# Optimization experiments

Hardware: AMD Instinct MI355X
Metric: run time of the kernel (lower is better)

The kernel has to match this reference:

```python
import jax, jax.numpy as jnp
import numpy as np

N_HEADS = 16

def setup_inputs() -> dict:
    key = jax.random.key(0)
    ks = jax.random.split(key, 8)
    bs, t, h, dh = 32, 512, 1024, 64
    s = lambda k, shape: jax.random.normal(k, shape, dtype=jnp.float32) * 0.02
    return {
        "x": jax.random.normal(ks[0], (bs, t, h), dtype=jnp.float32),
        "Wq": s(ks[1], (h, h)),
        "bq": s(ks[2], (h,)),
        "Wk": s(ks[3], (h, h)),
        "bk": s(ks[4], (h,)),
        "Wv": s(ks[5], (h, dh)),
        "bv": s(ks[6], (dh,)),
        "Wo": s(ks[7], (dh, h)),
    }

def reference(x, Wq, bq, Wk, bk, Wv, bv, Wo):
    bs, t, h = x.shape
    dh = Wv.shape[1]
    nh = N_HEADS
    # projections (context == x; static_features=None path)
    q = (x @ Wq + bq).reshape(bs, t, nh, dh)   # [b,t,h,d]
    k = (x @ Wk + bk).reshape(bs, t, nh, dh)
    v = x @ Wv + bv                             # shared single-head V: [b,t,d]
    scale = dh ** -0.5
    # per-head scores [b,h,q,k]
    score = jnp.einsum('bqhd,bkhd->bhqk', q, k) * scale
    # causal mask (mask_future_timesteps=True): -inf above diagonal
    mask = jnp.triu(jnp.full((t, t), -jnp.inf, dtype=score.dtype), 1)
    score = score + mask
    prob = jax.nn.softmax(score, axis=-1)       # attn_dropout is identity (p=0)
    # broadcast shared V across heads
    attn_vec = jnp.einsum('bhqk,bkd->bhqd', prob, v)   # [b,h,t,d]
    m_attn_vec = jnp.mean(attn_vec, axis=1)            # head-mean pooling [b,t,d]
    out = m_attn_vec @ Wo                              # out_proj, no bias; out_dropout identity
    return out, attn_vec
```

## Files before the change

kernel.cpp:

```cpp
#include <hip/hip_runtime.h>
#include <hip/hip_bf16.h>
#include <math.h>

#define BS 32
#define TT 512
#define HH 1024
#define NH 16
#define DH 64
#define MM (BS*TT)
#define NCAT 2176

typedef __attribute__((ext_vector_type(8))) __bf16 bf16x8;
typedef __attribute__((ext_vector_type(4))) float  f32x4;

#define QSCALE 0.18033688011112042f

#if __has_builtin(__builtin_amdgcn_exp2f)
#define EXP2F(x) __builtin_amdgcn_exp2f(x)
#else
#define EXP2F(x) __expf((x) * 0.69314718055994531f)
#endif

__device__ __forceinline__ void gld16(const void* g, void* l) {
    __builtin_amdgcn_global_load_lds(
        (const __attribute__((address_space(1))) unsigned int*)g,
        (__attribute__((address_space(3))) unsigned int*)l,
        16, 0, 0);
}

__global__ __launch_bounds__(256) void cvt_x(const float* __restrict__ x,
                                             __bf16* __restrict__ xb)
{
    const size_t i = ((size_t)blockIdx.x * 256 + threadIdx.x) * 8;
    float4 a = *(const float4*)(x + i);
    float4 b = *(const float4*)(x + i + 4);
    bf16x8 v;
    v[0] = (__bf16)a.x; v[1] = (__bf16)a.y; v[2] = (__bf16)a.z; v[3] = (__bf16)a.w;
    v[4] = (__bf16)b.x; v[5] = (__bf16)b.y; v[6] = (__bf16)b.z; v[7] = (__bf16)b.w;
    *(bf16x8*)(xb + i) = v;
}

__global__ __launch_bounds__(256) void prep_w(
    const float* __restrict__ Wq, const float* __restrict__ Wk,
    const float* __restrict__ Wv, const float* __restrict__ bq_,
    const float* __restrict__ bk_, const float* __restrict__ bv_,
    __bf16* __restrict__ Wt, float* __restrict__ bias_cat)
{
    __shared__ __align__(16) __bf16 tile[64][72];
    const int tid = threadIdx.x;
    const int n0 = blockIdx.x * 64;
    const int k0 = blockIdx.y * 64;

    const int n_l = tid & 63;
    const int k_b = tid >> 6;
    const int n   = n0 + n_l;
    #pragma unroll
    for (int j = 0; j < 16; ++j) {
        const int k_l = j * 4 + k_b;
        const int k   = k0 + k_l;
        float v;
        if (n < 1024)      v = Wq[(size_t)k * 1024 + n];
        else if (n < 2048) v = Wk[(size_t)k * 1024 + (n - 1024)];
        else if (n < 2112) v = Wv[(size_t)k * 64 + (n - 2048)];
        else               v = 0.f;
        tile[n_l][k_l] = (__bf16)v;
    }
    if (blockIdx.y == 0 && tid < 64) {
        const int nn = n0 + tid;
        bias_cat[nn] = (nn < 1024) ? bq_[nn]
                     : (nn < 2048) ? bk_[nn - 1024]
                     : (nn < 2112) ? bv_[nn - 2048] : 0.f;
    }
    __syncthreads();
    const int n_l2 = tid >> 2;
    const int k_l2 = (tid & 3) * 16;
    __bf16* dst = Wt + (size_t)(n0 + n_l2) * 1024 + k0 + k_l2;
    *(bf16x8*)dst       = *(const bf16x8*)&tile[n_l2][k_l2];
    *(bf16x8*)(dst + 8) = *(const bf16x8*)&tile[n_l2][k_l2 + 8];
}

__global__ __launch_bounds__(256) void gemm_qkv(
    const __bf16* __restrict__ A, const __bf16* __restrict__ B,
    const float* __restrict__ bias_cat,
    __bf16* __restrict__ Qo, __bf16* __restrict__ Ko,
    __bf16* __restrict__ Vt)
{
    __shared__ __align__(16) __bf16 sA[128 * 32];
    __shared__ __align__(16) __bf16 sB[128 * 32];

    const int tid  = threadIdx.x;
    const int wv   = tid >> 6;
    const int ln   = tid & 63;
    const int quad = ln >> 4;
    const int l16  = ln & 15;

    const int orig = blockIdx.y * 17 + blockIdx.x;
    const int swz  = (orig & 7) * 272 + (orig >> 3);
    const int m0 = (swz / 17) * 128;
    const int n0 = (swz % 17) * 128;

    const int rw = (wv & 1) * 64;
    const int cw = (wv >> 1) * 64;

    f32x4 acc[4][4];
    #pragma unroll
    for (int i = 0; i < 4; ++i)
        #pragma unroll
        for (int j = 0; j < 4; ++j) acc[i][j] = f32x4{0, 0, 0, 0};

    const int srow = wv * 16 + (ln >> 2);
    const int scol = (ln & 3) * 8;
    const __bf16* ga0 = A + (size_t)(m0 + srow) * 1024 + scol;
    const __bf16* gb0 = B + (size_t)(n0 + srow) * 1024 + scol;
    __bf16* la0 = sA + wv * 512;
    __bf16* lb0 = sB + wv * 512;

    for (int k0 = 0; k0 < 1024; k0 += 32) {
        gld16(ga0 + k0, la0);
        gld16(ga0 + (size_t)64 * 1024 + k0, la0 + 2048);
        gld16(gb0 + k0, lb0);
        gld16(gb0 + (size_t)64 * 1024 + k0, lb0 + 2048);
        __syncthreads();

        bf16x8 af[4], bfr[4];
        #pragma unroll
        for (int mt = 0; mt < 4; ++mt)
            af[mt] = *(const bf16x8*)&sA[(rw + mt * 16 + l16) * 32 + quad * 8];
        #pragma unroll
        for (int nt = 0; nt < 4; ++nt)
            bfr[nt] = *(const bf16x8*)&sB[(cw + nt * 16 + l16) * 32 + quad * 8];
        #pragma unroll
        for (int mt = 0; mt < 4; ++mt)
            #pragma unroll
            for (int nt = 0; nt < 4; ++nt)
                acc[mt][nt] = __builtin_amdgcn_mfma_f32_16x16x32_bf16(af[mt], bfr[nt], acc[mt][nt], 0, 0, 0);
        __syncthreads();
    }

    #pragma unroll
    for (int mt = 0; mt < 4; ++mt) {
        #pragma unroll
        for (int nt = 0; nt < 4; ++nt) {
            const int colb = n0 + cw + nt * 16 + l16;
            if (colb >= 2112) continue;
            const float bias = bias_cat[colb];
            #pragma unroll
            for (int r = 0; r < 4; ++r) {
                const int row = m0 + rw + mt * 16 + quad * 4 + r;
                const int b = row >> 9, t = row & 511;
                float v = acc[mt][nt][r] + bias;
                if (colb < 1024) {
                    const int h = colb >> 6, d = colb & 63;
                    Qo[(((size_t)(b * NH + h) * TT) + t) * DH + d] = (__bf16)(v * QSCALE);
                } else if (colb < 2048) {
                    const int c = colb - 1024;
                    const int h = c >> 6, d = c & 63;
                    Ko[(((size_t)(b * NH + h) * TT) + t) * DH + d] = (__bf16)v;
                } else {
                    const int d = colb - 2048;
                    Vt[((size_t)(b * DH + d)) * TT + t] = (__bf16)v;
                }
            }
        }
    }
}

__global__ __launch_bounds__(1024) void attn_mfma(
    const __bf16* __restrict__ Q, const __bf16* __restrict__ K,
    const __bf16* __restrict__ Vt, float* __restrict__ attn_vec)
{
    __shared__ __align__(16) __bf16 sK[512 * 64];
    __shared__ __align__(16) __bf16 sV[64][512];

    const int bh   = blockIdx.x;
    const int b    = bh >> 4;
    const int wave = threadIdx.x >> 6;
    const int lane = threadIdx.x & 63;
    const int quad = lane >> 4;
    const int l16  = lane & 15;

    const int s_ = wave & 3, j_ = wave >> 2;
    const int qt2 = (j_ == 0) ? s_ : (j_ == 1) ? (7 - s_) : (j_ == 2) ? (8 + s_) : (15 - s_);
    const int q0   = qt2 << 5;
    const int kend = q0 + 32;

    const __bf16* Qbh = Q + (size_t)bh * TT * DH;
    const __bf16* Kbh = K + (size_t)bh * TT * DH;
    const __bf16* Vb  = Vt + (size_t)b * DH * TT;

    #pragma unroll
    for (int r = 0; r < 4; ++r) {
        const int c   = wave * 4 + r;
        const int row = c * 8 + (lane >> 3);
        const int p   = lane & 7;
        const int swz = (row & 3) | (((row >> 3) & 1) << 2);
        gld16(Kbh + (size_t)row * DH + ((p ^ swz) * 8), sK + (size_t)c * 512);
    }
    const int svw = wave & 7;
    #pragma unroll
    for (int r = 0; r < 4; ++r) {
        const int row = wave + r * 16;
        gld16(Vb + (size_t)row * TT + ((lane ^ svw) * 8), &sV[row][0]);
    }

    const bf16x8 qA_lo = *(const bf16x8*)(Qbh + (size_t)(q0 + l16) * DH + quad * 8);
    const bf16x8 qA_hi = *(const bf16x8*)(Qbh + (size_t)(q0 + l16) * DH + 32 + quad * 8);
    const bf16x8 qB_lo = *(const bf16x8*)(Qbh + (size_t)(q0 + 16 + l16) * DH + quad * 8);
    const bf16x8 qB_hi = *(const bf16x8*)(Qbh + (size_t)(q0 + 16 + l16) * DH + 32 + quad * 8);

    const int perm = ((l16 >> 2) << 3) + (l16 & 3);
    const int swzl = (l16 & 3) | (((l16 >> 2) & 1) << 2);
    const __bf16* k1lo = sK + (size_t)perm * DH       + (( quad      ^ swzl) * 8);
    const __bf16* k1hi = sK + (size_t)perm * DH       + (((quad | 4) ^ swzl) * 8);
    const __bf16* k2lo = sK + (size_t)(perm + 4) * DH + (( quad      ^ swzl) * 8);
    const __bf16* k2hi = sK + (size_t)(perm + 4) * DH + (((quad | 4) ^ swzl) * 8);

    const int sx = l16 & 7;

    f32x4 OA[4] = {f32x4{0,0,0,0}, f32x4{0,0,0,0}, f32x4{0,0,0,0}, f32x4{0,0,0,0}};
    f32x4 OB[4] = {f32x4{0,0,0,0}, f32x4{0,0,0,0}, f32x4{0,0,0,0}, f32x4{0,0,0,0}};
    float lA = 0.f, lB = 0.f;

    __syncthreads();

    for (int kb0 = 0; kb0 < kend; kb0 += 32) {
        const int ko = kb0 * DH;
        bf16x8 c1a = *(const bf16x8*)(k1lo + ko);
        bf16x8 c1b = *(const bf16x8*)(k1hi + ko);
        bf16x8 c2a = *(const bf16x8*)(k2lo + ko);
        bf16x8 c2b = *(const bf16x8*)(k2hi + ko);

        const int vg = (((kb0 >> 3) + quad) ^ sx) * 8;
        bf16x8 vf0 = *(const bf16x8*)&sV[l16][vg];
        bf16x8 vf1 = *(const bf16x8*)&sV[16 + l16][vg];
        bf16x8 vf2 = *(const bf16x8*)&sV[32 + l16][vg];
        bf16x8 vf3 = *(const bf16x8*)&sV[48 + l16][vg];

        f32x4 s1A = __builtin_amdgcn_mfma_f32_16x16x32_bf16(c1a, qA_lo, f32x4{0,0,0,0}, 0, 0, 0);
        s1A       = __builtin_amdgcn_mfma_f32_16x16x32_bf16(c1b, qA_hi, s1A, 0, 0, 0);
        f32x4 s2A = __builtin_amdgcn_mfma_f32_16x16x32_bf16(c2a, qA_lo, f32x4{0,0,0,0}, 0, 0, 0);
        s2A       = __builtin_amdgcn_mfma_f32_16x16x32_bf16(c2b, qA_hi, s2A, 0, 0, 0);
        f32x4 s1B = __builtin_amdgcn_mfma_f32_16x16x32_bf16(c1a, qB_lo, f32x4{0,0,0,0}, 0, 0, 0);
        s1B       = __builtin_amdgcn_mfma_f32_16x16x32_bf16(c1b, qB_hi, s1B, 0, 0, 0);
        f32x4 s2B = __builtin_amdgcn_mfma_f32_16x16x32_bf16(c2a, qB_lo, f32x4{0,0,0,0}, 0, 0, 0);
        s2B       = __builtin_amdgcn_mfma_f32_16x16x32_bf16(c2b, qB_hi, s2B, 0, 0, 0);

        if (kb0 == q0) {
            const int qqA = q0 + l16, qqB = q0 + 16 + l16;
            #pragma unroll
            for (int r = 0; r < 4; ++r) {
                const int key1 = kb0 + quad * 8 + r;
                const int key2 = key1 + 4;
                if (key1 > qqA) s1A[r] = -INFINITY;
                if (key2 > qqA) s2A[r] = -INFINITY;
                if (key1 > qqB) s1B[r] = -INFINITY;
                if (key2 > qqB) s2B[r] = -INFINITY;
            }
        }

        bf16x8 pfA, pfB;
        float psA0 = 0.f, psA1 = 0.f, psB0 = 0.f, psB1 = 0.f;
        #pragma unroll
        for (int r = 0; r < 4; ++r) {
            float pa0 = EXP2F(s1A[r]);
            float pa1 = EXP2F(s2A[r]);
            float pb0 = EXP2F(s1B[r]);
            float pb1 = EXP2F(s2B[r]);
            psA0 += pa0; psA1 += pa1;
            psB0 += pb0; psB1 += pb1;
            pfA[r]     = (__bf16)pa0;
            pfA[4 + r] = (__bf16)pa1;
            pfB[r]     = (__bf16)pb0;
            pfB[4 + r] = (__bf16)pb1;
        }
        lA += psA0 + psA1;
        lB += psB0 + psB1;

        OA[0] = __builtin_amdgcn_mfma_f32_16x16x32_bf16(pfA, vf0, OA[0], 0, 0, 0);
        OB[0] = __builtin_amdgcn_mfma_f32_16x16x32_bf16(pfB, vf0, OB[0], 0, 0, 0);
        OA[1] = __builtin_amdgcn_mfma_f32_16x16x32_bf16(pfA, vf1, OA[1], 0, 0, 0);
        OB[1] = __builtin_amdgcn_mfma_f32_16x16x32_bf16(pfB, vf1, OB[1], 0, 0, 0);
        OA[2] = __builtin_amdgcn_mfma_f32_16x16x32_bf16(pfA, vf2, OA[2], 0, 0, 0);
        OB[2] = __builtin_amdgcn_mfma_f32_16x16x32_bf16(pfB, vf2, OB[2], 0, 0, 0);
        OA[3] = __builtin_amdgcn_mfma_f32_16x16x32_bf16(pfA, vf3, OA[3], 0, 0, 0);
        OB[3] = __builtin_amdgcn_mfma_f32_16x16x32_bf16(pfB, vf3, OB[3], 0, 0, 0);
    }

    lA += __shfl_xor(lA, 16);
    lA += __shfl_xor(lA, 32);
    lB += __shfl_xor(lB, 16);
    lB += __shfl_xor(lB, 32);

    #pragma unroll
    for (int r = 0; r < 4; ++r) {
        const float invA = 1.0f / __shfl(lA, quad * 4 + r);
        const float invB = 1.0f / __shfl(lB, quad * 4 + r);
        const int tA = q0 + quad * 4 + r;
        const int tB = tA + 16;
        float* opA = attn_vec + ((size_t)bh * TT + tA) * DH + l16;
        float* opB = attn_vec + ((size_t)bh * TT + tB) * DH + l16;
        #pragma unroll
        for (int nt = 0; nt < 4; ++nt) {
            opA[nt * 16] = OA[nt][r] * invA;
            opB[nt * 16] = OB[nt][r] * invB;
        }
    }
}

__global__ __launch_bounds__(256) void reduce_heads(
    const float* __restrict__ av, float* __restrict__ mav)
{
    const size_t idx = (size_t)blockIdx.x * 256 + threadIdx.x;
    const int    d4  = (int)(idx & 15);
    const size_t bt  = idx >> 4;
    const int    b   = (int)(bt >> 9);
    const int    t   = (int)(bt & 511);
    const float4* p = (const float4*)av + (((size_t)b * NH * TT) + t) * 16 + d4;
    float4 a = p[0];
    #pragma unroll
    for (int h = 1; h < NH; ++h) {
        float4 v = p[(size_t)h * TT * 16];
        a.x += v.x; a.y += v.y; a.z += v.z; a.w += v.w;
    }
    float4 o;
    o.x = a.x * (1.f / 16.f); o.y = a.y * (1.f / 16.f);
    o.z = a.z * (1.f / 16.f); o.w = a.w * (1.f / 16.f);
    ((float4*)mav)[idx] = o;
}

__global__ __launch_bounds__(256) void gemm_out(
    const float* __restrict__ A, const float* __restrict__ B,
    float* __restrict__ C, int M, int N, int K)
{
    __shared__ __align__(16) __bf16 sA[64][32];
    __shared__ __align__(16) __bf16 sB[64][32];

    const int tid  = threadIdx.x;
    const int wave = tid >> 6;
    const int lane = tid & 63;
    const int m0 = blockIdx.y * 64;
    const int n0 = blockIdx.x * 64;

    f32x4 acc[4] = {f32x4{0,0,0,0}, f32x4{0,0,0,0}, f32x4{0,0,0,0}, f32x4{0,0,0,0}};

    const int ar = tid >> 2;
    const int ac = (tid & 3) * 8;
    const int bk = tid >> 3;
    const int bc = (tid & 7) * 8;
    const int quad = lane >> 4;
    const int l16  = lane & 15;

    for (int k0 = 0; k0 < K; k0 += 32) {
        const float* ap = A + (size_t)(m0 + ar) * K + k0 + ac;
        float4 a0 = *(const float4*)ap;
        float4 a1 = *(const float4*)(ap + 4);
        {
            bf16x8 av;
            av[0] = (__bf16)a0.x; av[1] = (__bf16)a0.y; av[2] = (__bf16)a0.z; av[3] = (__bf16)a0.w;
            av[4] = (__bf16)a1.x; av[5] = (__bf16)a1.y; av[6] = (__bf16)a1.z; av[7] = (__bf16)a1.w;
            *(bf16x8*)&sA[ar][ac] = av;
        }
        const float* bp = B + (size_t)(k0 + bk) * N + n0 + bc;
        float4 b0 = *(const float4*)bp;
        float4 b1 = *(const float4*)(bp + 4);
        sB[bc + 0][bk] = (__bf16)b0.x;
        sB[bc + 1][bk] = (__bf16)b0.y;
        sB[bc + 2][bk] = (__bf16)b0.z;
        sB[bc + 3][bk] = (__bf16)b0.w;
        sB[bc + 4][bk] = (__bf16)b1.x;
        sB[bc + 5][bk] = (__bf16)b1.y;
        sB[bc + 6][bk] = (__bf16)b1.z;
        sB[bc + 7][bk] = (__bf16)b1.w;
        __syncthreads();

        bf16x8 afrag = *(const bf16x8*)&sA[wave * 16 + l16][quad * 8];
        #pragma unroll
        for (int tn = 0; tn < 4; ++tn) {
            bf16x8 bfrag = *(const bf16x8*)&sB[tn * 16 + l16][quad * 8];
            acc[tn] = __builtin_amdgcn_mfma_f32_16x16x32_bf16(afrag, bfrag, acc[tn], 0, 0, 0);
        }
        __syncthreads();
    }

    #pragma unroll
    for (int tn = 0; tn < 4; ++tn) {
        #pragma unroll
        for (int r = 0; r < 4; ++r) {
            int row = m0 + wave * 16 + quad * 4 + r;
            int col = n0 + tn * 16 + l16;
            C[(size_t)row * N + col] = acc[tn][r];
        }
    }
}

extern "C" void kernel_launch(void* const* d_in, const int* in_sizes, int n_in,
                              void* d_out, int out_size, void* d_ws, size_t ws_size,
                              hipStream_t stream)
{
    const float* x  = (const float*)d_in[0];
    const float* Wq = (const float*)d_in[1];
    const float* bq = (const float*)d_in[2];
    const float* Wk = (const float*)d_in[3];
    const float* bk = (const float*)d_in[4];
    const float* Wv = (const float*)d_in[5];
    const float* bv = (const float*)d_in[6];
    const float* Wo = (const float*)d_in[7];

    float* out      = (float*)d_out;
    float* attn_vec = out + (size_t)MM * HH;

    char* ws = (char*)d_ws;
    __bf16* xb  = (__bf16*)ws;
    __bf16* Wt  = xb + (size_t)MM * HH;
    float* bias_cat = (float*)(Wt + (size_t)NCAT * HH);
    __bf16* Qb  = (__bf16*)(bias_cat + 2304);
    __bf16* Kb  = Qb + (size_t)MM * HH;
    __bf16* Vt  = Kb + (size_t)MM * HH;
    float*  mav = (float*)xb;

    cvt_x<<<MM * HH / (256 * 8), 256, 0, stream>>>(x, xb);
    prep_w<<<dim3(NCAT / 64, HH / 64), 256, 0, stream>>>(Wq, Wk, Wv, bq, bk, bv, Wt, bias_cat);
    gemm_qkv<<<dim3(NCAT / 128, MM / 128), 256, 0, stream>>>(xb, Wt, bias_cat, Qb, Kb, Vt);
    attn_mfma<<<BS * NH, 1024, 0, stream>>>(Qb, Kb, Vt, attn_vec);
    reduce_heads<<<(MM * DH / 4) / 256, 256, 0, stream>>>(attn_vec, mav);
    gemm_out<<<dim3(HH / 64, MM / 64), 256, 0, stream>>>(mav, Wo, out, MM, HH, DH);
}
```

Measured before the change: 359.2 us.

## Double-buffer QKV GEMM with BK=64 swizzled LDS and rework output projection

The QKV GEMM now uses a K-step of 64 with XOR-swizzled LDS tiles and double buffering, so the next tile's global-to-LDS loads are issued while MFMAs run on the current tile, with one barrier per step. The head-mean reduction now writes bf16 directly, and Wo is pre-transposed to bf16 in a new small kernel. The output GEMM reads fragments straight from global memory without LDS and computes a larger 64x64 tile per wave. This adds LDS usage, which may lower occupancy in the QKV GEMM, and an extra launch.

```diff
diff --git a/kernel.cpp b/kernel.cpp
--- a/kernel.cpp
+++ b/kernel.cpp
@@ -79,14 +79,26 @@
     *(bf16x8*)(dst + 8) = *(const bf16x8*)&tile[n_l2][k_l2 + 8];
 }
 
+__global__ __launch_bounds__(256) void prep_wo(const float* __restrict__ Wo,
+                                               __bf16* __restrict__ WoT)
+{
+    const int idx = blockIdx.x * 256 + threadIdx.x;
+    const int n  = idx >> 3;
+    const int k0 = (idx & 7) * 8;
+    bf16x8 v;
+    #pragma unroll
+    for (int j = 0; j < 8; ++j) v[j] = (__bf16)Wo[(size_t)(k0 + j) * 1024 + n];
+    *(bf16x8*)(WoT + (size_t)n * 64 + k0) = v;
+}
+
 __global__ __launch_bounds__(256) void gemm_qkv(
     const __bf16* __restrict__ A, const __bf16* __restrict__ B,
     const float* __restrict__ bias_cat,
     __bf16* __restrict__ Qo, __bf16* __restrict__ Ko,
     __bf16* __restrict__ Vt)
 {
-    __shared__ __align__(16) __bf16 sA[128 * 32];
-    __shared__ __align__(16) __bf16 sB[128 * 32];
+    __shared__ __align__(16) __bf16 sA[2][128 * 64];
+    __shared__ __align__(16) __bf16 sB[2][128 * 64];
 
     const int tid  = threadIdx.x;
     const int wv   = tid >> 6;
@@ -108,33 +120,52 @@
         #pragma unroll
         for (int j = 0; j < 4; ++j) acc[i][j] = f32x4{0, 0, 0, 0};
 
-    const int srow = wv * 16 + (ln >> 2);
-    const int scol = (ln & 3) * 8;
-    const __bf16* ga0 = A + (size_t)(m0 + srow) * 1024 + scol;
-    const __bf16* gb0 = B + (size_t)(n0 + srow) * 1024 + scol;
-    __bf16* la0 = sA + wv * 512;
-    __bf16* lb0 = sB + wv * 512;
-
-    for (int k0 = 0; k0 < 1024; k0 += 32) {
-        gld16(ga0 + k0, la0);
-        gld16(ga0 + (size_t)64 * 1024 + k0, la0 + 2048);
-        gld16(gb0 + k0, lb0);
-        gld16(gb0 + (size_t)64 * 1024 + k0, lb0 + 2048);
+    const int srow8 = ln >> 3;
+    const int srcg  = (ln & 7) ^ (srow8 & 7);
+    const int swr   = (l16 & 7);
+
+    #pragma unroll
+    for (int r = 0; r < 4; ++r) {
+        const int rowb = wv * 32 + r * 8;
+        gld16(A + (size_t)(m0 + rowb + srow8) * 1024 + srcg * 8, &sA[0][rowb * 64]);
+        gld16(B + (size_t)(n0 + rowb + srow8) * 1024 + srcg * 8, &sB[0][rowb * 64]);
+    }
+    __syncthreads();
+
+    int p = 0;
+    for (int k0 = 0; k0 < 1024; k0 += 64) {
+        if (k0 + 64 < 1024) {
+            #pragma unroll
+            for (int r = 0; r < 4; ++r) {
+                const int rowb = wv * 32 + r * 8;
+                gld16(A + (size_t)(m0 + rowb + srow8) * 1024 + k0 + 64 + srcg * 8,
+                      &sA[p ^ 1][rowb * 64]);
+                gld16(B + (size_t)(n0 + rowb + srow8) * 1024 + k0 + 64 + srcg * 8,
+                      &sB[p ^ 1][rowb * 64]);
+            }
+        }
+        __builtin_amdgcn_sched_barrier(0);
+
+        const __bf16* la = sA[p];
+        const __bf16* lb = sB[p];
+        #pragma unroll
+        for (int ks = 0; ks < 2; ++ks) {
+            const int pg = ((ks * 4 + quad) ^ swr) * 8;
+            bf16x8 af[4], bfr[4];
+            #pragma unroll
+            for (int mt = 0; mt < 4; ++mt)
+                af[mt] = *(const bf16x8*)&la[(rw + mt * 16 + l16) * 64 + pg];
+            #pragma unroll
+            for (int nt = 0; nt < 4; ++nt)
+                bfr[nt] = *(const bf16x8*)&lb[(cw + nt * 16 + l16) * 64 + pg];
+            #pragma unroll
+            for (int mt = 0; mt < 4; ++mt)
+                #pragma unroll
+                for (int nt = 0; nt < 4; ++nt)
+                    acc[mt][nt] = __builtin_amdgcn_mfma_f32_16x16x32_bf16(af[mt], bfr[nt], acc[mt][nt], 0, 0, 0);
+        }
         __syncthreads();
-
-        bf16x8 af[4], bfr[4];
-        #pragma unroll
-        for (int mt = 0; mt < 4; ++mt)
-            af[mt] = *(const bf16x8*)&sA[(rw + mt * 16 + l16) * 32 + quad * 8];
-        #pragma unroll
-        for (int nt = 0; nt < 4; ++nt)
-            bfr[nt] = *(const bf16x8*)&sB[(cw + nt * 16 + l16) * 32 + quad * 8];
-        #pragma unroll
-        for (int mt = 0; mt < 4; ++mt)
-            #pragma unroll
-            for (int nt = 0; nt < 4; ++nt)
-                acc[mt][nt] = __builtin_amdgcn_mfma_f32_16x16x32_bf16(af[mt], bfr[nt], acc[mt][nt], 0, 0, 0);
-        __syncthreads();
+        p ^= 1;
     }
 
     #pragma unroll
@@ -192,9 +223,9 @@
     for (int r = 0; r < 4; ++r) {
         const int c   = wave * 4 + r;
         const int row = c * 8 + (lane >> 3);
-        const int p   = lane & 7;
-        const int swz = (row & 3) | (((row >> 3) & 1) << 2);
-        gld16(Kbh + (size_t)row * DH + ((p ^ swz) * 8), sK + (size_t)c * 512);
+        const int pp  = lane & 7;
+        const int swzr = (row & 3) | (((row >> 3) & 1) << 2);
+        gld16(Kbh + (size_t)row * DH + ((pp ^ swzr) * 8), sK + (size_t)c * 512);
     }
     const int svw = wave & 7;
     #pragma unroll
@@ -308,87 +339,74 @@
 }
 
 __global__ __launch_bounds__(256) void reduce_heads(
-    const float* __restrict__ av, float* __restrict__ mav)
+    const float* __restrict__ av, __bf16* __restrict__ mavb)
 {
     const size_t idx = (size_t)blockIdx.x * 256 + threadIdx.x;
-    const int    d4  = (int)(idx & 15);
-    const size_t bt  = idx >> 4;
+    const int    d8  = (int)(idx & 7) * 8;
+    const size_t bt  = idx >> 3;
     const int    b   = (int)(bt >> 9);
     const int    t   = (int)(bt & 511);
-    const float4* p = (const float4*)av + (((size_t)b * NH * TT) + t) * 16 + d4;
-    float4 a = p[0];
+    const float4* p = (const float4*)av + ((size_t)b * NH * TT + t) * 16 + (d8 >> 2);
+    float4 a0 = p[0], a1 = p[1];
     #pragma unroll
     for (int h = 1; h < NH; ++h) {
-        float4 v = p[(size_t)h * TT * 16];
-        a.x += v.x; a.y += v.y; a.z += v.z; a.w += v.w;
-    }
-    float4 o;
-    o.x = a.x * (1.f / 16.f); o.y = a.y * (1.f / 16.f);
-    o.z = a.z * (1.f / 16.f); o.w = a.w * (1.f / 16.f);
-    ((float4*)mav)[idx] = o;
+        const float4* q = p + (size_t)h * TT * 16;
+        float4 v0 = q[0], v1 = q[1];
+        a0.x += v0.x; a0.y += v0.y; a0.z += v0.z; a0.w += v0.w;
+        a1.x += v1.x; a1.y += v1.y; a1.z += v1.z; a1.w += v1.w;
+    }
+    bf16x8 o;
+    o[0] = (__bf16)(a0.x * (1.f/16.f)); o[1] = (__bf16)(a0.y * (1.f/16.f));
+    o[2] = (__bf16)(a0.z * (1.f/16.f)); o[3] = (__bf16)(a0.w * (1.f/16.f));
+    o[4] = (__bf16)(a1.x * (1.f/16.f)); o[5] = (__bf16)(a1.y * (1.f/16.f));
+    o[6] = (__bf16)(a1.z * (1.f/16.f)); o[7] = (__bf16)(a1.w * (1.f/16.f));
+    *(bf16x8*)(mavb + bt * DH + d8) = o;
 }
 
 __global__ __launch_bounds__(256) void gemm_out(
-    const float* __restrict__ A, const float* __restrict__ B,
-    float* __restrict__ C, int M, int N, int K)
-{
-    __shared__ __align__(16) __bf16 sA[64][32];
-    __shared__ __align__(16) __bf16 sB[64][32];
-
+    const __bf16* __restrict__ A, const __bf16* __restrict__ Bt,
+    float* __restrict__ C)
+{
     const int tid  = threadIdx.x;
-    const int wave = tid >> 6;
-    const int lane = tid & 63;
-    const int m0 = blockIdx.y * 64;
+    const int wv   = tid >> 6;
+    const int ln   = tid & 63;
+    const int quad = ln >> 4;
+    const int l16  = ln & 15;
     const int n0 = blockIdx.x * 64;
-
-    f32x4 acc[4] = {f32x4{0,0,0,0}, f32x4{0,0,0,0}, f32x4{0,0,0,0}, f32x4{0,0,0,0}};
-
-    const int ar = tid >> 2;
-    const int ac = (tid & 3) * 8;
-    const int bk = tid >> 3;
-    const int bc = (tid & 7) * 8;
-    const int quad = lane >> 4;
-    const int l16  = lane & 15;
-
-    for (int k0 = 0; k0 < K; k0 += 32) {
-        const float* ap = A + (size_t)(m0 + ar) * K + k0 + ac;
-        float4 a0 = *(const float4*)ap;
-        float4 a1 = *(const float4*)(ap + 4);
-        {
-            bf16x8 av;
-            av[0] = (__bf16)a0.x; av[1] = (__bf16)a0.y; av[2] = (__bf16)a0.z; av[3] = (__bf16)a0.w;
-            av[4] = (__bf16)a1.x; av[5] = (__bf16)a1.y; av[6] = (__bf16)a1.z; av[7] = (__bf16)a1.w;
-            *(bf16x8*)&sA[ar][ac] = av;
-        }
-        const float* bp = B + (size_t)(k0 + bk) * N + n0 + bc;
-        float4 b0 = *(const float4*)bp;
-        float4 b1 = *(const float4*)(bp + 4);
-        sB[bc + 0][bk] = (__bf16)b0.x;
-        sB[bc + 1][bk] = (__bf16)b0.y;
-        sB[bc + 2][bk] = (__bf16)b0.z;
-        sB[bc + 3][bk] = (__bf16)b0.w;
-        sB[bc + 4][bk] = (__bf16)b1.x;
-        sB[bc + 5][bk] = (__bf16)b1.y;
-        sB[bc + 6][bk] = (__bf16)b1.z;
-        sB[bc + 7][bk] = (__bf16)b1.w;
-        __syncthreads();
-
-        bf16x8 afrag = *(const bf16x8*)&sA[wave * 16 + l16][quad * 8];
-        #pragma unroll
-        for (int tn = 0; tn < 4; ++tn) {
-            bf16x8 bfrag = *(const bf16x8*)&sB[tn * 16 + l16][quad * 8];
-            acc[tn] = __builtin_amdgcn_mfma_f32_16x16x32_bf16(afrag, bfrag, acc[tn], 0, 0, 0);
-        }
-        __syncthreads();
-    }
-
-    #pragma unroll
-    for (int tn = 0; tn < 4; ++tn) {
-        #pragma unroll
-        for (int r = 0; r < 4; ++r) {
-            int row = m0 + wave * 16 + quad * 4 + r;
-            int col = n0 + tn * 16 + l16;
-            C[(size_t)row * N + col] = acc[tn][r];
+    const int m0 = blockIdx.y * 256 + wv * 64;
+
+    f32x4 acc[4][4];
+    #pragma unroll
+    for (int i = 0; i < 4; ++i)
+        #pragma unroll
+        for (int j = 0; j < 4; ++j) acc[i][j] = f32x4{0, 0, 0, 0};
+
+    #pragma unroll
+    for (int ks = 0; ks < 2; ++ks) {
+        const int kofs = ks * 32 + quad * 8;
+        bf16x8 bfr[4];
+        #pragma unroll
+        for (int nt = 0; nt < 4; ++nt)
+            bfr[nt] = *(const bf16x8*)&Bt[(size_t)(n0 + nt * 16 + l16) * 64 + kofs];
+        #pragma unroll
+        for (int mt = 0; mt < 4; ++mt) {
+            bf16x8 af = *(const bf16x8*)&A[(size_t)(m0 + mt * 16 + l16) * 64 + kofs];
+            #pragma unroll
+            for (int nt = 0; nt < 4; ++nt)
+                acc[mt][nt] = __builtin_amdgcn_mfma_f32_16x16x32_bf16(af, bfr[nt], acc[mt][nt], 0, 0, 0);
+        }
+    }
+
+    #pragma unroll
+    for (int mt = 0; mt < 4; ++mt) {
+        #pragma unroll
+        for (int nt = 0; nt < 4; ++nt) {
+            #pragma unroll
+            for (int r = 0; r < 4; ++r) {
+                const int row = m0 + mt * 16 + quad * 4 + r;
+                const int col = n0 + nt * 16 + l16;
+                C[(size_t)row * HH + col] = acc[mt][nt][r];
+            }
         }
     }
 }
@@ -416,12 +434,14 @@
     __bf16* Qb  = (__bf16*)(bias_cat + 2304);
     __bf16* Kb  = Qb + (size_t)MM * HH;
     __bf16* Vt  = Kb + (size_t)MM * HH;
-    float*  mav = (float*)xb;
+    __bf16* WoT = Vt + (size_t)BS * DH * TT;
+    __bf16* mavb = xb;
 
     cvt_x<<<MM * HH / (256 * 8), 256, 0, stream>>>(x, xb);
     prep_w<<<dim3(NCAT / 64, HH / 64), 256, 0, stream>>>(Wq, Wk, Wv, bq, bk, bv, Wt, bias_cat);
+    prep_wo<<<(HH * 8) / 256, 256, 0, stream>>>(Wo, WoT);
     gemm_qkv<<<dim3(NCAT / 128, MM / 128), 256, 0, stream>>>(xb, Wt, bias_cat, Qb, Kb, Vt);
     attn_mfma<<<BS * NH, 1024, 0, stream>>>(Qb, Kb, Vt, attn_vec);
-    reduce_heads<<<(MM * DH / 4) / 256, 256, 0, stream>>>(attn_vec, mav);
-    gemm_out<<<dim3(HH / 64, MM / 64), 256, 0, stream>>>(mav, Wo, out, MM, HH, DH);
-}
+    reduce_heads<<<(MM * 8) / 256, 256, 0, stream>>>(attn_vec, mavb);
+    gemm_out<<<dim3(HH / 64, MM / 256), 256, 0, stream>>>(mavb, WoT, out);
+}
```

Measured after the change: 376.3 us. 1.05x slower.
